# Kernel optimization log

Hardware: AMD Instinct MI355X
Metric: run time of the kernel (lower is better)

Reference implementation:

```python
import jax, jax.numpy as jnp
import numpy as np

TEMPERATURE = 0.5
EPS = 1e-8  # torch CosineSimilarity eps


def setup_inputs() -> dict:
    key = jax.random.key(0)
    k1, k2, k3 = jax.random.split(key, 3)
    N, D, C = 8192, 128, 1000
    embed = jax.random.normal(k1, (N, D), dtype=jnp.float32)
    proxy = jax.random.normal(k2, (N, D), dtype=jnp.float32)
    label = jax.random.randint(k3, (N,), 0, C, dtype=jnp.int64)
    return {"embed": embed, "proxy": proxy, "label": label}


def _l2_normalize(x):
    # mirrors torch CosineSimilarity: x / max(||x||, eps)
    n = jnp.sqrt(jnp.sum(x * x, axis=-1, keepdims=True))
    return x / jnp.maximum(n, EPS)


def reference(embed, proxy, label):
    N = embed.shape[0]
    en = _l2_normalize(embed)                       # [N, D]
    # pairwise cosine sim via normalize+matmul (instead of O(N^2 D) broadcast)
    sim = jnp.exp(jnp.einsum("nd,md->nm", en, en) / TEMPERATURE)  # [N, N]
    offdiag = 1.0 - jnp.eye(N, dtype=sim.dtype)
    sim = sim * offdiag                             # zero diag == remove-diag for row sums
    # positives: same label, excluding self
    same = (label[:, None] == label[None, :]).astype(sim.dtype) * offdiag
    pos_sum = jnp.sum(sim * same, axis=1)           # [N]
    # embed-to-proxy similarity
    pn = _l2_normalize(proxy)
    emb2proxy = jnp.exp(jnp.sum(en * pn, axis=-1) / TEMPERATURE)  # [N]
    numerator = emb2proxy + pos_sum
    denominator = emb2proxy + jnp.sum(sim, axis=1)
    return -jnp.mean(jnp.log(numerator / denominator))
```

## Files before the change

### kernel.cpp

```cpp
#include <hip/hip_runtime.h>
#include <hip/hip_bf16.h>

#define N_ROWS 8192
#define DIM    128
#define NCHUNK 16
#define CHUNKC (N_ROWS / NCHUNK)
#define NT     (CHUNKC / 32)
#define NPH    (NT / 2)

#define ENSCALE 1.6986436f

typedef __attribute__((ext_vector_type(8)))  short short8;
typedef __attribute__((ext_vector_type(16))) float f32x16;
typedef __attribute__((address_space(3))) void lds_void;
typedef const __attribute__((address_space(1))) void g_void;

__device__ inline unsigned short f2bf(float f) {
    unsigned u = __float_as_uint(f);
    unsigned r = (u + 0x7FFFu + ((u >> 16) & 1u)) >> 16;
    return (unsigned short)r;
}
__device__ inline float bf2f(unsigned short u) {
    return __uint_as_float(((unsigned)u) << 16);
}
__device__ inline int labof(int4 v, int j) {
    return j == 0 ? v.x : j == 1 ? v.y : j == 2 ? v.z : v.w;
}

__global__ __launch_bounds__(256) void norm_kernel(
    const float* __restrict__ embed, const float* __restrict__ proxy,
    short* __restrict__ enb, float* __restrict__ e2p)
{
    int wave = threadIdx.x >> 6, lane = threadIdx.x & 63;
    int row = blockIdx.x * 4 + wave;

    const float2 ev = *(const float2*)(embed + row * DIM + lane * 2);
    float ss = ev.x * ev.x + ev.y * ev.y;
#pragma unroll
    for (int m = 1; m < 64; m <<= 1) ss += __shfl_xor(ss, m, 64);
    float inv_e = 1.0f / fmaxf(sqrtf(ss), 1e-8f);
    float ex = ev.x * inv_e, ey = ev.y * inv_e;

    const float2 pv = *(const float2*)(proxy + row * DIM + lane * 2);
    float ps = pv.x * pv.x + pv.y * pv.y;
#pragma unroll
    for (int m = 1; m < 64; m <<= 1) ps += __shfl_xor(ps, m, 64);
    float inv_p = 1.0f / fmaxf(sqrtf(ps), 1e-8f);

    float dot = ex * (pv.x * inv_p) + ey * (pv.y * inv_p);
#pragma unroll
    for (int m = 1; m < 64; m <<= 1) dot += __shfl_xor(dot, m, 64);

    ushort2 st; st.x = f2bf(ex * ENSCALE); st.y = f2bf(ey * ENSCALE);
    *(ushort2*)(enb + row * DIM + lane * 2) = st;
    if (lane == 0) e2p[row] = __expf(2.0f * dot);
}

#define DOTILE(buf, tt, cb_tile)                                               \
    {                                                                          \
        const char* base_ = lds + (buf) * 16384 + (tt) * 8192 + cl * 256;      \
        short8 b[8];                                                           \
        _Pragma("unroll")                                                      \
        for (int kk = 0; kk < 8; kk++) {                                       \
            int off = ((kk * 2 + hi) ^ (cl & 15)) * 16;                        \
            b[kk] = *(const short8*)(base_ + off);                             \
        }                                                                      \
        f32x16 c0 = {}, c1 = {};                                               \
        __builtin_amdgcn_s_setprio(1);                                         \
        _Pragma("unroll")                                                      \
        for (int kk = 0; kk < 8; kk++) {                                       \
            c0 = __builtin_amdgcn_mfma_f32_32x32x16_bf16(b[kk], rres0[kk], c0, \
                                                         0, 0, 0);             \
            c1 = __builtin_amdgcn_mfma_f32_32x32x16_bf16(b[kk], rres1[kk], c1, \
                                                         0, 0, 0);             \
        }                                                                      \
        __builtin_amdgcn_s_setprio(0);                                         \
        const bool d0_ = ((cb_tile) == wrbase);                                \
        const bool d1_ = ((cb_tile) == wrbase + 32);                           \
        _Pragma("unroll")                                                      \
        for (int r = 0; r < 16; r++) {                                         \
            int colr = (r & 3) + 4 * hi + 8 * (r >> 2);                        \
            float s0 = __builtin_amdgcn_exp2f(c0[r]);                          \
            float s1 = __builtin_amdgcn_exp2f(c1[r]);                          \
            s0 = (d0_ && colr == cl) ? 0.f : s0;                               \
            s1 = (d1_ && colr == cl) ? 0.f : s1;                               \
            tot0[r & 3] += s0;                                                 \
            tot1[r & 3] += s1;                                                 \
        }                                                                      \
    }

__global__ __launch_bounds__(256, 2) void simsum_kernel(
    const short* __restrict__ enb, float* __restrict__ ptot)
{
    __shared__ __align__(16) char lds[3 * 16384];
    const int tid = threadIdx.x;
    const int wave = tid >> 6;
    const int lane = tid & 63;
    const int cl = lane & 31;
    const int hi = lane >> 5;
    const int wrbase = blockIdx.x * 256 + wave * 64;
    const int cbase0 = blockIdx.y * CHUNKC;

    const int sc = tid >> 4;
    const int sj = (tid & 15) ^ sc;

    auto stage = [&](int buf, int ph) {
        const int cb = cbase0 + ph * 64;
        char* dbase = lds + buf * 16384 + wave * 1024;
#pragma unroll
        for (int h = 0; h < 4; h++) {
            const short* src = enb + (size_t)(cb + h * 16 + sc) * DIM + sj * 8;
            __builtin_amdgcn_global_load_lds((g_void*)src,
                                             (lds_void*)(dbase + h * 4096),
                                             16, 0, 0);
        }
    };

    short8 rres0[8], rres1[8];
    {
        const short* a0 = enb + (size_t)(wrbase + cl) * DIM + hi * 8;
        const short* a1 = enb + (size_t)(wrbase + 32 + cl) * DIM + hi * 8;
#pragma unroll
        for (int kk = 0; kk < 8; kk++) {
            rres0[kk] = *(const short8*)(a0 + kk * 16);
            rres1[kk] = *(const short8*)(a1 + kk * 16);
        }
    }

    float tot0[4] = {0.f, 0.f, 0.f, 0.f};
    float tot1[4] = {0.f, 0.f, 0.f, 0.f};

    stage(0, 0);
    stage(1, 1);

#pragma unroll 1
    for (int ph = 0; ph < NPH; ph++) {
        if (ph < NPH - 1) {
            asm volatile("s_waitcnt vmcnt(4)" ::: "memory");
        } else {
            asm volatile("s_waitcnt vmcnt(0)" ::: "memory");
        }
        __builtin_amdgcn_s_barrier();
        if (ph + 2 < NPH) stage((ph + 2) % 3, ph + 2);

        const int buf = ph % 3;
        const int cb = cbase0 + ph * 64;
        DOTILE(buf, 0, cb);
        DOTILE(buf, 1, cb + 32);
    }

    float t0 = tot0[0] + tot0[1] + tot0[2] + tot0[3];
    float t1 = tot1[0] + tot1[1] + tot1[2] + tot1[3];
    t0 += __shfl_xor(t0, 32, 64);
    t1 += __shfl_xor(t1, 32, 64);
    if (hi == 0) {
        ptot[blockIdx.y * N_ROWS + wrbase + cl] = t0;
        ptot[blockIdx.y * N_ROWS + wrbase + 32 + cl] = t1;
    }
}

__global__ __launch_bounds__(256) void pos_kernel(
    const short* __restrict__ enb, const int* __restrict__ label,
    float* __restrict__ posr)
{
    int wave = threadIdx.x >> 6, lane = threadIdx.x & 63;
    int row = blockIdx.x * 4 + wave;
    int mylab = label[row];

    ushort2 e2 = *(const ushort2*)(enb + (size_t)row * DIM + lane * 2);
    float ei0 = bf2f(e2.x), ei1 = bf2f(e2.y);

    float acc = 0.f;
#pragma unroll 1
    for (int ch = 0; ch < N_ROWS / 256; ch++) {
        int4 lv = *(const int4*)(label + ch * 256 + lane * 4);
#pragma unroll
        for (int q = 0; q < 4; q++) {
            int j = ch * 256 + lane * 4 + q;
            bool m = (labof(lv, q) == mylab) && (j != row);
            unsigned long long mask = __ballot(m);
            while (mask) {
                int jj = ch * 256 + 4 * (__ffsll(mask) - 1) + q;
                mask &= mask - 1;
                ushort2 f2 = *(const ushort2*)(enb + (size_t)jj * DIM + lane * 2);
                float d = ei0 * bf2f(f2.x) + ei1 * bf2f(f2.y);
#pragma unroll
                for (int s = 1; s < 64; s <<= 1) d += __shfl_xor(d, s, 64);
                acc += __builtin_amdgcn_exp2f(d);
            }
        }
    }
    if (lane == 0) posr[row] = acc;
}

__global__ __launch_bounds__(256) void loss_partial_kernel(
    const float* __restrict__ e2p, const float* __restrict__ ptot,
    const float* __restrict__ posr, float* __restrict__ pl)
{
    int i = blockIdx.x * 256 + threadIdx.x;
    float tot = 0.f;
#pragma unroll
    for (int c = 0; c < NCHUNK; c++) tot += ptot[c * N_ROWS + i];
    float e = e2p[i];
    float v = __logf((e + posr[i]) / (e + tot));
#pragma unroll
    for (int m = 1; m < 64; m <<= 1) v += __shfl_xor(v, m, 64);
    __shared__ float red[4];
    int wave = threadIdx.x >> 6, lane = threadIdx.x & 63;
    if (lane == 0) red[wave] = v;
    __syncthreads();
    if (threadIdx.x == 0) pl[blockIdx.x] = red[0] + red[1] + red[2] + red[3];
}

__global__ void loss_final_kernel(const float* __restrict__ pl,
                                  float* __restrict__ out)
{
    float v = (threadIdx.x < 32) ? pl[threadIdx.x] : 0.f;
#pragma unroll
    for (int m = 1; m < 64; m <<= 1) v += __shfl_xor(v, m, 64);
    if (threadIdx.x == 0) out[0] = -v / (float)N_ROWS;
}

extern "C" void kernel_launch(void* const* d_in, const int* in_sizes, int n_in,
                              void* d_out, int out_size, void* d_ws, size_t ws_size,
                              hipStream_t stream) {
    const float* embed = (const float*)d_in[0];
    const float* proxy = (const float*)d_in[1];
    const int*   label = (const int*)d_in[2];
    float* out = (float*)d_out;

    char* ws = (char*)d_ws;
    short* enb  = (short*)ws;
    float* e2p  = (float*)(ws + 2u * N_ROWS * DIM);
    float* ptot = e2p + N_ROWS;
    float* posr = ptot + NCHUNK * N_ROWS;
    float* pl   = posr + N_ROWS;

    hipLaunchKernelGGL(norm_kernel, dim3(N_ROWS / 4), dim3(256), 0, stream,
                       embed, proxy, enb, e2p);
    hipLaunchKernelGGL(simsum_kernel, dim3(N_ROWS / 256, NCHUNK), dim3(256), 0, stream,
                       enb, ptot);
    hipLaunchKernelGGL(pos_kernel, dim3(N_ROWS / 4), dim3(256), 0, stream,
                       enb, label, posr);
    hipLaunchKernelGGL(loss_partial_kernel, dim3(N_ROWS / 256), dim3(256), 0, stream,
                       e2p, ptot, posr, pl);
    hipLaunchKernelGGL(loss_final_kernel, dim3(1), dim3(64), 0, stream, pl, out);
}
```

Before: 54.87 us.

## Shrink simsum tiles for higher occupancy and fuse positive-sum with loss reduction

The similarity-sum kernel now processes one 32-column tile per pipeline phase instead of two. That cuts LDS to 24 KB and raises the launch-bounds occupancy target from 2 to 4 blocks per CU, while the column chunk count doubles to 32 so there are more blocks. The positive-pair kernel is merged with the per-row loss partial computation, which removes one launch and the posr round trip. The final reduction is widened to 256 threads to sum the 2048 per-block partials. The cost is twice as many ptot partials to read and more barrier-per-MFMA overhead per phase.

```diff
diff --git a/kernel.cpp b/kernel.cpp
--- a/kernel.cpp
+++ b/kernel.cpp
@@ -3,10 +3,9 @@
 
 #define N_ROWS 8192
 #define DIM    128
-#define NCHUNK 16
+#define NCHUNK 32
 #define CHUNKC (N_ROWS / NCHUNK)
-#define NT     (CHUNKC / 32)
-#define NPH    (NT / 2)
+#define NPH    (CHUNKC / 32)
 
 #define ENSCALE 1.6986436f
 
@@ -56,43 +55,10 @@
     if (lane == 0) e2p[row] = __expf(2.0f * dot);
 }
 
-#define DOTILE(buf, tt, cb_tile)                                               \
-    {                                                                          \
-        const char* base_ = lds + (buf) * 16384 + (tt) * 8192 + cl * 256;      \
-        short8 b[8];                                                           \
-        _Pragma("unroll")                                                      \
-        for (int kk = 0; kk < 8; kk++) {                                       \
-            int off = ((kk * 2 + hi) ^ (cl & 15)) * 16;                        \
-            b[kk] = *(const short8*)(base_ + off);                             \
-        }                                                                      \
-        f32x16 c0 = {}, c1 = {};                                               \
-        __builtin_amdgcn_s_setprio(1);                                         \
-        _Pragma("unroll")                                                      \
-        for (int kk = 0; kk < 8; kk++) {                                       \
-            c0 = __builtin_amdgcn_mfma_f32_32x32x16_bf16(b[kk], rres0[kk], c0, \
-                                                         0, 0, 0);             \
-            c1 = __builtin_amdgcn_mfma_f32_32x32x16_bf16(b[kk], rres1[kk], c1, \
-                                                         0, 0, 0);             \
-        }                                                                      \
-        __builtin_amdgcn_s_setprio(0);                                         \
-        const bool d0_ = ((cb_tile) == wrbase);                                \
-        const bool d1_ = ((cb_tile) == wrbase + 32);                           \
-        _Pragma("unroll")                                                      \
-        for (int r = 0; r < 16; r++) {                                         \
-            int colr = (r & 3) + 4 * hi + 8 * (r >> 2);                        \
-            float s0 = __builtin_amdgcn_exp2f(c0[r]);                          \
-            float s1 = __builtin_amdgcn_exp2f(c1[r]);                          \
-            s0 = (d0_ && colr == cl) ? 0.f : s0;                               \
-            s1 = (d1_ && colr == cl) ? 0.f : s1;                               \
-            tot0[r & 3] += s0;                                                 \
-            tot1[r & 3] += s1;                                                 \
-        }                                                                      \
-    }
-
-__global__ __launch_bounds__(256, 2) void simsum_kernel(
+__global__ __launch_bounds__(256, 4) void simsum_kernel(
     const short* __restrict__ enb, float* __restrict__ ptot)
 {
-    __shared__ __align__(16) char lds[3 * 16384];
+    __shared__ __align__(16) char lds[3 * 8192];
     const int tid = threadIdx.x;
     const int wave = tid >> 6;
     const int lane = tid & 63;
@@ -102,13 +68,13 @@
     const int cbase0 = blockIdx.y * CHUNKC;
 
     const int sc = tid >> 4;
-    const int sj = (tid & 15) ^ sc;
-
-    auto stage = [&](int buf, int ph) {
-        const int cb = cbase0 + ph * 64;
-        char* dbase = lds + buf * 16384 + wave * 1024;
-#pragma unroll
-        for (int h = 0; h < 4; h++) {
+    const int sj = (tid & 15) ^ (sc & 15);
+
+    auto stage = [&](int buf, int t) {
+        const int cb = cbase0 + t * 32;
+        char* dbase = lds + buf * 8192 + wave * 1024;
+#pragma unroll
+        for (int h = 0; h < 2; h++) {
             const short* src = enb + (size_t)(cb + h * 16 + sc) * DIM + sj * 8;
             __builtin_amdgcn_global_load_lds((g_void*)src,
                                              (lds_void*)(dbase + h * 4096),
@@ -136,7 +102,7 @@
 #pragma unroll 1
     for (int ph = 0; ph < NPH; ph++) {
         if (ph < NPH - 1) {
-            asm volatile("s_waitcnt vmcnt(4)" ::: "memory");
+            asm volatile("s_waitcnt vmcnt(2)" ::: "memory");
         } else {
             asm volatile("s_waitcnt vmcnt(0)" ::: "memory");
         }
@@ -144,9 +110,37 @@
         if (ph + 2 < NPH) stage((ph + 2) % 3, ph + 2);
 
         const int buf = ph % 3;
-        const int cb = cbase0 + ph * 64;
-        DOTILE(buf, 0, cb);
-        DOTILE(buf, 1, cb + 32);
+        const int cb = cbase0 + ph * 32;
+
+        const char* base_ = lds + buf * 8192 + cl * 256;
+        short8 b[8];
+#pragma unroll
+        for (int kk = 0; kk < 8; kk++) {
+            int off = ((kk * 2 + hi) ^ (cl & 15)) * 16;
+            b[kk] = *(const short8*)(base_ + off);
+        }
+
+        f32x16 c0 = {}, c1 = {};
+        __builtin_amdgcn_s_setprio(1);
+#pragma unroll
+        for (int kk = 0; kk < 8; kk++) {
+            c0 = __builtin_amdgcn_mfma_f32_32x32x16_bf16(b[kk], rres0[kk], c0, 0, 0, 0);
+            c1 = __builtin_amdgcn_mfma_f32_32x32x16_bf16(b[kk], rres1[kk], c1, 0, 0, 0);
+        }
+        __builtin_amdgcn_s_setprio(0);
+
+        const bool d0_ = (cb == wrbase);
+        const bool d1_ = (cb == wrbase + 32);
+#pragma unroll
+        for (int r = 0; r < 16; r++) {
+            int colr = (r & 3) + 4 * hi + 8 * (r >> 2);
+            float s0 = __builtin_amdgcn_exp2f(c0[r]);
+            float s1 = __builtin_amdgcn_exp2f(c1[r]);
+            s0 = (d0_ && colr == cl) ? 0.f : s0;
+            s1 = (d1_ && colr == cl) ? 0.f : s1;
+            tot0[r & 3] += s0;
+            tot1[r & 3] += s1;
+        }
     }
 
     float t0 = tot0[0] + tot0[1] + tot0[2] + tot0[3];
@@ -159,9 +153,10 @@
     }
 }
 
-__global__ __launch_bounds__(256) void pos_kernel(
+__global__ __launch_bounds__(256) void posloss_kernel(
     const short* __restrict__ enb, const int* __restrict__ label,
-    float* __restrict__ posr)
+    const float* __restrict__ e2p, const float* __restrict__ ptot,
+    float* __restrict__ pl)
 {
     int wave = threadIdx.x >> 6, lane = threadIdx.x & 63;
     int row = blockIdx.x * 4 + wave;
@@ -190,35 +185,33 @@
             }
         }
     }
-    if (lane == 0) posr[row] = acc;
-}
-
-__global__ __launch_bounds__(256) void loss_partial_kernel(
-    const float* __restrict__ e2p, const float* __restrict__ ptot,
-    const float* __restrict__ posr, float* __restrict__ pl)
-{
-    int i = blockIdx.x * 256 + threadIdx.x;
+
     float tot = 0.f;
 #pragma unroll
-    for (int c = 0; c < NCHUNK; c++) tot += ptot[c * N_ROWS + i];
-    float e = e2p[i];
-    float v = __logf((e + posr[i]) / (e + tot));
+    for (int c = 0; c < NCHUNK; c++) tot += ptot[c * N_ROWS + row];
+    float e = e2p[row];
+    float v = __logf((e + acc) / (e + tot));
+
+    __shared__ float red[4];
+    if (lane == 0) red[wave] = v;
+    __syncthreads();
+    if (threadIdx.x == 0) pl[blockIdx.x] = red[0] + red[1] + red[2] + red[3];
+}
+
+__global__ __launch_bounds__(256) void loss_final_kernel(
+    const float* __restrict__ pl, float* __restrict__ out)
+{
+    float v = 0.f;
+#pragma unroll
+    for (int q = 0; q < 8; q++) v += pl[threadIdx.x * 8 + q];
 #pragma unroll
     for (int m = 1; m < 64; m <<= 1) v += __shfl_xor(v, m, 64);
     __shared__ float red[4];
     int wave = threadIdx.x >> 6, lane = threadIdx.x & 63;
     if (lane == 0) red[wave] = v;
     __syncthreads();
-    if (threadIdx.x == 0) pl[blockIdx.x] = red[0] + red[1] + red[2] + red[3];
-}
-
-__global__ void loss_final_kernel(const float* __restrict__ pl,
-                                  float* __restrict__ out)
-{
-    float v = (threadIdx.x < 32) ? pl[threadIdx.x] : 0.f;
-#pragma unroll
-    for (int m = 1; m < 64; m <<= 1) v += __shfl_xor(v, m, 64);
-    if (threadIdx.x == 0) out[0] = -v / (float)N_ROWS;
+    if (threadIdx.x == 0)
+        out[0] = -(red[0] + red[1] + red[2] + red[3]) / (float)N_ROWS;
 }
 
 extern "C" void kernel_launch(void* const* d_in, const int* in_sizes, int n_in,
@@ -233,16 +226,13 @@
     short* enb  = (short*)ws;
     float* e2p  = (float*)(ws + 2u * N_ROWS * DIM);
     float* ptot = e2p + N_ROWS;
-    float* posr = ptot + NCHUNK * N_ROWS;
-    float* pl   = posr + N_ROWS;
+    float* pl   = ptot + NCHUNK * N_ROWS;
 
     hipLaunchKernelGGL(norm_kernel, dim3(N_ROWS / 4), dim3(256), 0, stream,
                        embed, proxy, enb, e2p);
     hipLaunchKernelGGL(simsum_kernel, dim3(N_ROWS / 256, NCHUNK), dim3(256), 0, stream,
                        enb, ptot);
-    hipLaunchKernelGGL(pos_kernel, dim3(N_ROWS / 4), dim3(256), 0, stream,
-                       enb, label, posr);
-    hipLaunchKernelGGL(loss_partial_kernel, dim3(N_ROWS / 256), dim3(256), 0, stream,
-                       e2p, ptot, posr, pl);
-    hipLaunchKernelGGL(loss_final_kernel, dim3(1), dim3(64), 0, stream, pl, out);
-}
+    hipLaunchKernelGGL(posloss_kernel, dim3(N_ROWS / 4), dim3(256), 0, stream,
+                       enb, label, e2p, ptot, pl);
+    hipLaunchKernelGGL(loss_final_kernel, dim3(1), dim3(256), 0, stream, pl, out);
+}
```

Result: slower. 82.67 us (+50.7%).

## Register-staged double-buffered simsum pipeline, more chunks, fuse pos and loss kernels

Applied to the files above, without the earlier changes.

The simsum kernel replaces the global_load_lds triple buffer with register-staged global loads written into a two-buffer LDS ring. It also halves the LDS footprint, raises the occupancy hint to 4 blocks and doubles the column chunk count to 32 for more parallelism. The positive-sum kernel now also reduces the per-chunk totals and computes the per-row log term, which removes one launch and the posr round trip. The final reduction is widened to 256 threads over 2048 partials. The trade-off is more register pressure, a barrier on every phase, and more partial sums to reduce.

```diff
diff --git a/kernel.cpp b/kernel.cpp
--- a/kernel.cpp
+++ b/kernel.cpp
@@ -3,17 +3,14 @@
 
 #define N_ROWS 8192
 #define DIM    128
-#define NCHUNK 16
+#define NCHUNK 32
 #define CHUNKC (N_ROWS / NCHUNK)
-#define NT     (CHUNKC / 32)
-#define NPH    (NT / 2)
+#define NPH    (CHUNKC / 32)
 
 #define ENSCALE 1.6986436f
 
 typedef __attribute__((ext_vector_type(8)))  short short8;
 typedef __attribute__((ext_vector_type(16))) float f32x16;
-typedef __attribute__((address_space(3))) void lds_void;
-typedef const __attribute__((address_space(1))) void g_void;
 
 __device__ inline unsigned short f2bf(float f) {
     unsigned u = __float_as_uint(f);
@@ -56,15 +53,45 @@
     if (lane == 0) e2p[row] = __expf(2.0f * dot);
 }
 
-#define DOTILE(buf, tt, cb_tile)                                               \
+__global__ __launch_bounds__(256, 4) void simsum_kernel(
+    const short* __restrict__ enb, float* __restrict__ ptot)
+{
+    __shared__ __align__(16) char lds[2 * 8192];
+    const int tid = threadIdx.x;
+    const int wave = tid >> 6;
+    const int lane = tid & 63;
+    const int cl = lane & 31;
+    const int hi = lane >> 5;
+    const int wrbase = blockIdx.x * 256 + wave * 64;
+    const int cbase0 = blockIdx.y * CHUNKC;
+
+    const int sc = tid >> 4;
+    const int sj = (tid & 15) ^ (sc & 15);
+    char* wr0 = lds + wave * 1024 + lane * 16;
+
+#define GLOAD(t, g)                                                            \
     {                                                                          \
-        const char* base_ = lds + (buf) * 16384 + (tt) * 8192 + cl * 256;      \
+        int t_ = (t) > NPH - 1 ? NPH - 1 : (t);                                \
+        const int cb_ = cbase0 + t_ * 32;                                      \
+        g##0 = *(const short8*)(enb + (size_t)(cb_ + sc) * DIM + sj * 8);      \
+        g##1 = *(const short8*)(enb + (size_t)(cb_ + 16 + sc) * DIM + sj * 8); \
+    }
+#define SWRITE(buf, g)                                                         \
+    {                                                                          \
+        *(short8*)(wr0 + (buf) * 8192) = g##0;                                 \
+        *(short8*)(wr0 + (buf) * 8192 + 4096) = g##1;                          \
+    }
+#define PHASE(buf, ph, gw, gl)                                                 \
+    {                                                                          \
+        const char* base_ = lds + (buf) * 8192 + cl * 256;                     \
         short8 b[8];                                                           \
         _Pragma("unroll")                                                      \
         for (int kk = 0; kk < 8; kk++) {                                       \
             int off = ((kk * 2 + hi) ^ (cl & 15)) * 16;                        \
             b[kk] = *(const short8*)(base_ + off);                             \
         }                                                                      \
+        SWRITE((buf) ^ 1, gw);        \
+        GLOAD((ph) + 2, gl);                     \
         f32x16 c0 = {}, c1 = {};                                               \
         __builtin_amdgcn_s_setprio(1);                                         \
         _Pragma("unroll")                                                      \
@@ -75,8 +102,9 @@
                                                          0, 0, 0);             \
         }                                                                      \
         __builtin_amdgcn_s_setprio(0);                                         \
-        const bool d0_ = ((cb_tile) == wrbase);                                \
-        const bool d1_ = ((cb_tile) == wrbase + 32);                           \
+        const int cb_ = cbase0 + (ph) * 32;                                    \
+        const bool d0_ = (cb_ == wrbase);                                      \
+        const bool d1_ = (cb_ == wrbase + 32);                                 \
         _Pragma("unroll")                                                      \
         for (int r = 0; r < 16; r++) {                                         \
             int colr = (r & 3) + 4 * hi + 8 * (r >> 2);                        \
@@ -87,34 +115,9 @@
             tot0[r & 3] += s0;                                                 \
             tot1[r & 3] += s1;                                                 \
         }                                                                      \
-    }
-
-__global__ __launch_bounds__(256, 2) void simsum_kernel(
-    const short* __restrict__ enb, float* __restrict__ ptot)
-{
-    __shared__ __align__(16) char lds[3 * 16384];
-    const int tid = threadIdx.x;
-    const int wave = tid >> 6;
-    const int lane = tid & 63;
-    const int cl = lane & 31;
-    const int hi = lane >> 5;
-    const int wrbase = blockIdx.x * 256 + wave * 64;
-    const int cbase0 = blockIdx.y * CHUNKC;
-
-    const int sc = tid >> 4;
-    const int sj = (tid & 15) ^ sc;
-
-    auto stage = [&](int buf, int ph) {
-        const int cb = cbase0 + ph * 64;
-        char* dbase = lds + buf * 16384 + wave * 1024;
-#pragma unroll
-        for (int h = 0; h < 4; h++) {
-            const short* src = enb + (size_t)(cb + h * 16 + sc) * DIM + sj * 8;
-            __builtin_amdgcn_global_load_lds((g_void*)src,
-                                             (lds_void*)(dbase + h * 4096),
-                                             16, 0, 0);
-        }
-    };
+        asm volatile("s_waitcnt lgkmcnt(0)" ::: "memory");                     \
+        __builtin_amdgcn_s_barrier();                                          \
+    }
 
     short8 rres0[8], rres1[8];
     {
@@ -130,23 +133,17 @@
     float tot0[4] = {0.f, 0.f, 0.f, 0.f};
     float tot1[4] = {0.f, 0.f, 0.f, 0.f};
 
-    stage(0, 0);
-    stage(1, 1);
+    short8 gA0, gA1, gB0, gB1;
+    GLOAD(0, gA);
+    GLOAD(1, gB);
+    SWRITE(0, gA);
+    asm volatile("s_waitcnt lgkmcnt(0)" ::: "memory");
+    __builtin_amdgcn_s_barrier();
 
 #pragma unroll 1
-    for (int ph = 0; ph < NPH; ph++) {
-        if (ph < NPH - 1) {
-            asm volatile("s_waitcnt vmcnt(4)" ::: "memory");
-        } else {
-            asm volatile("s_waitcnt vmcnt(0)" ::: "memory");
-        }
-        __builtin_amdgcn_s_barrier();
-        if (ph + 2 < NPH) stage((ph + 2) % 3, ph + 2);
-
-        const int buf = ph % 3;
-        const int cb = cbase0 + ph * 64;
-        DOTILE(buf, 0, cb);
-        DOTILE(buf, 1, cb + 32);
+    for (int i = 0; i < NPH / 2; i++) {
+        PHASE(0, 2 * i,     gB, gA);
+        PHASE(1, 2 * i + 1, gA, gB);
     }
 
     float t0 = tot0[0] + tot0[1] + tot0[2] + tot0[3];
@@ -157,11 +154,15 @@
         ptot[blockIdx.y * N_ROWS + wrbase + cl] = t0;
         ptot[blockIdx.y * N_ROWS + wrbase + 32 + cl] = t1;
     }
-}
-
-__global__ __launch_bounds__(256) void pos_kernel(
+#undef GLOAD
+#undef SWRITE
+#undef PHASE
+}
+
+__global__ __launch_bounds__(256) void posloss_kernel(
     const short* __restrict__ enb, const int* __restrict__ label,
-    float* __restrict__ posr)
+    const float* __restrict__ e2p, const float* __restrict__ ptot,
+    float* __restrict__ pl)
 {
     int wave = threadIdx.x >> 6, lane = threadIdx.x & 63;
     int row = blockIdx.x * 4 + wave;
@@ -169,6 +170,8 @@
 
     ushort2 e2 = *(const ushort2*)(enb + (size_t)row * DIM + lane * 2);
     float ei0 = bf2f(e2.x), ei1 = bf2f(e2.y);
+
+    float tp = (lane < NCHUNK) ? ptot[lane * N_ROWS + row] : 0.f;
 
     float acc = 0.f;
 #pragma unroll 1
@@ -190,35 +193,33 @@
             }
         }
     }
-    if (lane == 0) posr[row] = acc;
-}
-
-__global__ __launch_bounds__(256) void loss_partial_kernel(
-    const float* __restrict__ e2p, const float* __restrict__ ptot,
-    const float* __restrict__ posr, float* __restrict__ pl)
-{
-    int i = blockIdx.x * 256 + threadIdx.x;
-    float tot = 0.f;
-#pragma unroll
-    for (int c = 0; c < NCHUNK; c++) tot += ptot[c * N_ROWS + i];
-    float e = e2p[i];
-    float v = __logf((e + posr[i]) / (e + tot));
+
+#pragma unroll
+    for (int m = 1; m < 64; m <<= 1) tp += __shfl_xor(tp, m, 64);
+
+    float e = e2p[row];
+    float v = __logf((e + acc) / (e + tp));
+
+    __shared__ float red[4];
+    if (lane == 0) red[wave] = v;
+    __syncthreads();
+    if (threadIdx.x == 0) pl[blockIdx.x] = red[0] + red[1] + red[2] + red[3];
+}
+
+__global__ __launch_bounds__(256) void loss_final_kernel(
+    const float* __restrict__ pl, float* __restrict__ out)
+{
+    float v = 0.f;
+#pragma unroll
+    for (int q = 0; q < 8; q++) v += pl[threadIdx.x * 8 + q];
 #pragma unroll
     for (int m = 1; m < 64; m <<= 1) v += __shfl_xor(v, m, 64);
     __shared__ float red[4];
     int wave = threadIdx.x >> 6, lane = threadIdx.x & 63;
     if (lane == 0) red[wave] = v;
     __syncthreads();
-    if (threadIdx.x == 0) pl[blockIdx.x] = red[0] + red[1] + red[2] + red[3];
-}
-
-__global__ void loss_final_kernel(const float* __restrict__ pl,
-                                  float* __restrict__ out)
-{
-    float v = (threadIdx.x < 32) ? pl[threadIdx.x] : 0.f;
-#pragma unroll
-    for (int m = 1; m < 64; m <<= 1) v += __shfl_xor(v, m, 64);
-    if (threadIdx.x == 0) out[0] = -v / (float)N_ROWS;
+    if (threadIdx.x == 0)
+        out[0] = -(red[0] + red[1] + red[2] + red[3]) / (float)N_ROWS;
 }
 
 extern "C" void kernel_launch(void* const* d_in, const int* in_sizes, int n_in,
@@ -233,16 +234,13 @@
     short* enb  = (short*)ws;
     float* e2p  = (float*)(ws + 2u * N_ROWS * DIM);
     float* ptot = e2p + N_ROWS;
-    float* posr = ptot + NCHUNK * N_ROWS;
-    float* pl   = posr + N_ROWS;
+    float* pl   = ptot + NCHUNK * N_ROWS;
 
     hipLaunchKernelGGL(norm_kernel, dim3(N_ROWS / 4), dim3(256), 0, stream,
                        embed, proxy, enb, e2p);
     hipLaunchKernelGGL(simsum_kernel, dim3(N_ROWS / 256, NCHUNK), dim3(256), 0, stream,
                        enb, ptot);
-    hipLaunchKernelGGL(pos_kernel, dim3(N_ROWS / 4), dim3(256), 0, stream,
-                       enb, label, posr);
-    hipLaunchKernelGGL(loss_partial_kernel, dim3(N_ROWS / 256), dim3(256), 0, stream,
-                       e2p, ptot, posr, pl);
-    hipLaunchKernelGGL(loss_final_kernel, dim3(1), dim3(64), 0, stream, pl, out);
-}
+    hipLaunchKernelGGL(posloss_kernel, dim3(N_ROWS / 4), dim3(256), 0, stream,
+                       enb, label, e2p, ptot, pl);
+    hipLaunchKernelGGL(loss_final_kernel, dim3(1), dim3(256), 0, stream, pl, out);
+}
```

New measurement: 84.65 us. 54.3% more time.
